# Kernel tuning notes

Measured on AMD Instinct MI355X. Metric: run time of the kernel, lower is better.

Reference implementation:

```python
import jax, jax.numpy as jnp
import numpy as np

N = 100000
E = 1600000
F_IN = 256
HID = 128
N_CLS = 2


def _glorot(k, shape):
    lim = float(np.sqrt(6.0 / (shape[0] + shape[1])))
    return jax.random.uniform(k, shape, jnp.float32, -lim, lim)


def setup_inputs() -> dict:
    key = jax.random.key(0)
    ks = jax.random.split(key, 10)
    x = jax.random.normal(ks[0], (N, F_IN), jnp.float32)
    edge_index = jax.random.randint(ks[1], (2, E), 0, N, dtype=jnp.int64)
    return {
        "x": x,
        "edge_index": edge_index,
        "W1": _glorot(ks[2], (F_IN, HID)), "b1": jnp.zeros((HID,), jnp.float32),
        "W2": _glorot(ks[3], (HID, HID)), "b2": jnp.zeros((HID,), jnp.float32),
        "W3": _glorot(ks[4], (HID, HID)), "b3": jnp.zeros((HID,), jnp.float32),
        "Wc": _glorot(ks[5], (HID, N_CLS)), "bc": jnp.zeros((N_CLS,), jnp.float32),
    }


def gcn_layer(x, W, b, src, dst, n):
    """PyG GCNConv: D^-1/2 (A+I) D^-1/2 X W + b with self-loops added."""
    xw = x @ W  # [N, H]
    # degree including the self-loop (all edge weights are 1)
    deg = jax.ops.segment_sum(jnp.ones((src.shape[0],), xw.dtype), dst,
                              num_segments=n) + 1.0
    dinv = jax.lax.rsqrt(deg)  # [N]
    norm = dinv[src] * dinv[dst]  # [E]
    msg = xw[src] * norm[:, None]  # [E, H] gathered+scaled messages
    out = jax.ops.segment_sum(msg, dst, num_segments=n)
    # self-loop contribution: norm = dinv[i]*dinv[i] = 1/deg[i]
    out = out + xw * (1.0 / deg)[:, None]
    return out + b


def reference(x, edge_index, W1, b1, W2, b2, W3, b3, Wc, bc):
    src, dst = edge_index[0], edge_index[1]
    h = jax.nn.relu(gcn_layer(x, W1, b1, src, dst, N))
    h = jax.nn.relu(gcn_layer(h, W2, b2, src, dst, N))  # dropout identity (eval)
    h = jax.nn.relu(gcn_layer(h, W3, b3, src, dst, N))
    logits = h @ Wc + bc  # [N, num_classes]
    return jax.nn.log_softmax(logits, axis=1)
```

## Files before the change

kernel.cpp:

```cpp
#include <hip/hip_runtime.h>
#include <hip/hip_bf16.h>
#include <cstdint>
#include <cstddef>

#define N_NODES 100000
#define N_EDGES 1600000
#define F_IN    256
#define HID     128
#define NB       ((N_NODES + 255) >> 8)
#define F3_CHUNK 7168
#define N_CHUNKS ((N_EDGES + F3_CHUNK - 1) / F3_CHUNK)

typedef __attribute__((ext_vector_type(8))) short  bf16x8;
typedef __attribute__((ext_vector_type(4))) float  f32x4;

static __device__ inline float bf2f(unsigned short u) {
    return __uint_as_float(((unsigned int)u) << 16);
}
static __device__ inline unsigned short f2bf(float f) {
    union { __hip_bfloat16 h; unsigned short u; } c;
    c.h = __float2bfloat16(f);
    return c.u;
}
static __device__ inline float lof(unsigned int w) { return __uint_as_float(w << 16); }
static __device__ inline float hif(unsigned int w) { return __uint_as_float(w & 0xffff0000u); }


__global__ __launch_bounds__(256) void zero_f_kernel(float* __restrict__ p, int n) {
    int i = blockIdx.x * 256 + threadIdx.x;
    if (i < n) p[i] = 0.f;
}


__global__ __launch_bounds__(256) void count_kernel(const int* __restrict__ dst,
                                                    int* __restrict__ ccnt, int nE) {
    __shared__ int c[NB];
    for (int i = threadIdx.x; i < NB; i += 256) c[i] = 0;
    __syncthreads();
    int base = blockIdx.x * F3_CHUNK;
    int m = min(F3_CHUNK, nE - base);
    for (int t = threadIdx.x; t < m; t += 256)
        atomicAdd(&c[dst[base + t] >> 8], 1);
    __syncthreads();
    for (int i = threadIdx.x; i < NB; i += 256)
        ccnt[i * N_CHUNKS + blockIdx.x] = c[i];
}


__global__ __launch_bounds__(256) void scanA_kernel(int* __restrict__ ccnt,
                                                    int* __restrict__ btot) {
    __shared__ int s[256];
    const int b = blockIdx.x;
    const int t = threadIdx.x;
    int v = (t < N_CHUNKS) ? ccnt[b * N_CHUNKS + t] : 0;
    s[t] = v;
    __syncthreads();
    for (int off = 1; off < 256; off <<= 1) {
        int add = (t >= off) ? s[t - off] : 0;
        __syncthreads();
        s[t] += add;
        __syncthreads();
    }
    if (t < N_CHUNKS) ccnt[b * N_CHUNKS + t] = s[t] - v;
    if (t == 255) btot[b] = s[255];
}


__global__ __launch_bounds__(512) void scanB_kernel(const int* __restrict__ btot,
                                                    int* __restrict__ bbase) {
    __shared__ int s[512];
    int t = threadIdx.x;
    int v = (t < NB) ? btot[t] : 0;
    s[t] = v;
    __syncthreads();
    for (int off = 1; off < 512; off <<= 1) {
        int add = (t >= off) ? s[t - off] : 0;
        __syncthreads();
        s[t] += add;
        __syncthreads();
    }
    if (t < NB) bbase[t] = s[t] - v;
    if (t == 0) bbase[NB] = N_EDGES;
}


__global__ __launch_bounds__(256) void stage_kernel(const int* __restrict__ src,
                                                    const int* __restrict__ dst,
                                                    const int* __restrict__ ccnt,
                                                    const int* __restrict__ bbase,
                                                    unsigned int* __restrict__ stg, int nE) {
    __shared__ int cnt[NB];
    __shared__ int bas[NB];
    const int chunk = blockIdx.x;
    for (int i = threadIdx.x; i < NB; i += 256) {
        cnt[i] = 0;
        bas[i] = bbase[i] + ccnt[i * N_CHUNKS + chunk];
    }
    __syncthreads();
    int base = chunk * F3_CHUNK;
    int m = min(F3_CHUNK, nE - base);
    for (int t = threadIdx.x; t < m; t += 256) {
        int d = dst[base + t];
        int s = src[base + t];
        int bkt = d >> 8;
        int k = atomicAdd(&cnt[bkt], 1);
        stg[bas[bkt] + k] = ((unsigned int)s << 8) | (unsigned int)(d & 255);
    }
}


__global__ __launch_bounds__(256) void bucket_finalize_kernel(
        const unsigned int* __restrict__ stg,
        const int* __restrict__ bbase,
        float* __restrict__ dinv,
        int* __restrict__ row_ptr,
        int* __restrict__ csr_src, int n) {
    __shared__ int c[256];
    __shared__ int s[256];
    __shared__ int lofs[256];
    const int b = blockIdx.x;
    const int t = threadIdx.x;
    const int beg = bbase[b], end = bbase[b + 1];

    c[t] = 0;
    __syncthreads();
    for (int i = beg + t; i < end; i += 256)
        atomicAdd(&c[stg[i] & 255u], 1);
    __syncthreads();

    const int node = b * 256 + t;
    const int myDeg = c[t];
    if (node < n) dinv[node] = rsqrtf((float)myDeg + 1.0f);

    s[t] = myDeg;
    __syncthreads();
    for (int off = 1; off < 256; off <<= 1) {
        int add = (t >= off) ? s[t - off] : 0;
        __syncthreads();
        s[t] += add;
        __syncthreads();
    }
    const int excl = s[t] - myDeg;
    lofs[t] = excl;
    if (node <= n) row_ptr[node] = beg + excl;

    __syncthreads();
    c[t] = 0;
    __syncthreads();
    for (int i = beg + t; i < end; i += 256) {
        unsigned int p = stg[i];
        int dl = (int)(p & 255u);
        int k = atomicAdd(&c[dl], 1);
        csr_src[beg + lofs[dl] + k] = (int)(p >> 8);
    }
}


static __device__ inline void blob_fill(const float* __restrict__ W,
                                        unsigned short* __restrict__ blob, int tid) {
    int lane = tid & 63;
    int c    = (tid >> 6) & 7;
    int s    = tid >> 9;
    int col  = c * 16 + (lane & 15);
    int kb   = s * 32 + (lane >> 4) * 8;
    bf16x8 o;
#pragma unroll
    for (int j = 0; j < 8; ++j)
        o[j] = (short)f2bf(W[(size_t)(kb + j) * HID + col]);
    *reinterpret_cast<bf16x8*>(blob + (size_t)tid * 8) = o;
}

__global__ __launch_bounds__(256) void prep_blob_all_kernel(const float* __restrict__ W1,
                                                            const float* __restrict__ W2,
                                                            const float* __restrict__ W3,
                                                            unsigned short* __restrict__ blob1,
                                                            unsigned short* __restrict__ blob2,
                                                            unsigned short* __restrict__ blob3) {
    int blk = blockIdx.x;
    if (blk < 16) {
        blob_fill(W1, blob1, blk * 256 + threadIdx.x);
    } else if (blk < 24) {
        blob_fill(W2, blob2, (blk - 16) * 256 + threadIdx.x);
    } else {
        blob_fill(W3, blob3, (blk - 24) * 256 + threadIdx.x);
    }
}


template <int K, bool IN_BF16>
__global__ __launch_bounds__(256) void mfma_gemm_kernel(const void* __restrict__ Xv,
                                                        const unsigned short* __restrict__ blob,
                                                        unsigned short* __restrict__ Y, int n) {
    constexpr int KSTEPS = K / 32;
    const int lane = threadIdx.x & 63;
    const int wave = threadIdx.x >> 6;
    const int rowbase = blockIdx.x * 128 + wave * 32;

    const int r0 = min(rowbase +      (lane & 15), n - 1);
    const int r1 = min(rowbase + 16 + (lane & 15), n - 1);
    const int koff = (lane >> 4) * 8;

    f32x4 acc0[8], acc1[8];
#pragma unroll
    for (int c = 0; c < 8; ++c) { acc0[c] = (f32x4)0.f; acc1[c] = (f32x4)0.f; }

#pragma unroll
    for (int s = 0; s < KSTEPS; ++s) {
        bf16x8 bfr[8];
#pragma unroll
        for (int c = 0; c < 8; ++c)
            bfr[c] = *reinterpret_cast<const bf16x8*>(blob + ((size_t)((s * 8 + c) * 64 + lane)) * 8);

        bf16x8 a0, a1;
        if (IN_BF16) {
            const unsigned short* Xb = (const unsigned short*)Xv;
            a0 = *reinterpret_cast<const bf16x8*>(Xb + (size_t)r0 * K + s * 32 + koff);
            a1 = *reinterpret_cast<const bf16x8*>(Xb + (size_t)r1 * K + s * 32 + koff);
        } else {
            const float* Xf = (const float*)Xv;
            const float4* p0 = reinterpret_cast<const float4*>(Xf + (size_t)r0 * K + s * 32 + koff);
            const float4* p1 = reinterpret_cast<const float4*>(Xf + (size_t)r1 * K + s * 32 + koff);
            float4 q0 = p0[0], q1 = p0[1], q2 = p1[0], q3 = p1[1];
            a0[0] = (short)f2bf(q0.x); a0[1] = (short)f2bf(q0.y);
            a0[2] = (short)f2bf(q0.z); a0[3] = (short)f2bf(q0.w);
            a0[4] = (short)f2bf(q1.x); a0[5] = (short)f2bf(q1.y);
            a0[6] = (short)f2bf(q1.z); a0[7] = (short)f2bf(q1.w);
            a1[0] = (short)f2bf(q2.x); a1[1] = (short)f2bf(q2.y);
            a1[2] = (short)f2bf(q2.z); a1[3] = (short)f2bf(q2.w);
            a1[4] = (short)f2bf(q3.x); a1[5] = (short)f2bf(q3.y);
            a1[6] = (short)f2bf(q3.z); a1[7] = (short)f2bf(q3.w);
        }

#pragma unroll
        for (int c = 0; c < 8; ++c) {
            acc0[c] = __builtin_amdgcn_mfma_f32_16x16x32_bf16(a0, bfr[c], acc0[c], 0, 0, 0);
            acc1[c] = __builtin_amdgcn_mfma_f32_16x16x32_bf16(a1, bfr[c], acc1[c], 0, 0, 0);
        }
    }

    const int col  = lane & 15;
    const int rsub = (lane >> 4) * 4;
#pragma unroll
    for (int c = 0; c < 8; ++c) {
#pragma unroll
        for (int r = 0; r < 4; ++r) {
            int row0 = rowbase + rsub + r;
            int row1 = rowbase + 16 + rsub + r;
            if (row0 < n) Y[(size_t)row0 * HID + c * 16 + col] = f2bf(acc0[c][r]);
            if (row1 < n) Y[(size_t)row1 * HID + c * 16 + col] = f2bf(acc1[c][r]);
        }
    }
}


template <bool CLS>
__global__ __launch_bounds__(256) void agg_gather_kernel(const unsigned short* __restrict__ xw,
                                                         const float* __restrict__ dinv,
                                                         const int* __restrict__ row_ptr,
                                                         const int* __restrict__ csr_src,
                                                         const float* __restrict__ b,
                                                         unsigned short* __restrict__ h,
                                                         const float* __restrict__ Wc,
                                                         const float* __restrict__ bc,
                                                         float* __restrict__ out, int n) {
    int v = (blockIdx.x * 256 + threadIdx.x) >> 6;
    if (v >= n) return;
    int lane = threadIdx.x & 63;

    int beg = __builtin_amdgcn_readfirstlane(row_ptr[v]);
    int end = __builtin_amdgcn_readfirstlane(row_ptr[v + 1]);

    const unsigned int* xw32 = (const unsigned int*)xw;
    float a0 = 0.f, a1 = 0.f;

    int j = beg;
    for (; j + 4 <= end; j += 4) {
        int s0 = __builtin_amdgcn_readfirstlane(csr_src[j + 0]);
        int s1 = __builtin_amdgcn_readfirstlane(csr_src[j + 1]);
        int s2 = __builtin_amdgcn_readfirstlane(csr_src[j + 2]);
        int s3 = __builtin_amdgcn_readfirstlane(csr_src[j + 3]);
        float d0 = dinv[s0], d1 = dinv[s1], d2 = dinv[s2], d3 = dinv[s3];
        unsigned int w0 = xw32[(size_t)s0 * 64 + lane];
        unsigned int w1 = xw32[(size_t)s1 * 64 + lane];
        unsigned int w2 = xw32[(size_t)s2 * 64 + lane];
        unsigned int w3 = xw32[(size_t)s3 * 64 + lane];
        a0 = fmaf(d0, lof(w0), a0); a1 = fmaf(d0, hif(w0), a1);
        a0 = fmaf(d1, lof(w1), a0); a1 = fmaf(d1, hif(w1), a1);
        a0 = fmaf(d2, lof(w2), a0); a1 = fmaf(d2, hif(w2), a1);
        a0 = fmaf(d3, lof(w3), a0); a1 = fmaf(d3, hif(w3), a1);
    }
    for (; j < end; ++j) {
        int s0 = __builtin_amdgcn_readfirstlane(csr_src[j]);
        float d0 = dinv[s0];
        unsigned int w0 = xw32[(size_t)s0 * 64 + lane];
        a0 = fmaf(d0, lof(w0), a0); a1 = fmaf(d0, hif(w0), a1);
    }

    float dv = dinv[v];
    unsigned int wv = xw32[(size_t)v * 64 + lane];
    float2 bb = *reinterpret_cast<const float2*>(b + 2 * lane);
    float s2v = dv * dv;
    float r0 = fmaxf(dv * a0 + s2v * lof(wv) + bb.x, 0.f);
    float r1 = fmaxf(dv * a1 + s2v * hif(wv) + bb.y, 0.f);

    if (!CLS) {
        unsigned int o = (unsigned int)f2bf(r0) | ((unsigned int)f2bf(r1) << 16);
        *reinterpret_cast<unsigned int*>(h + (size_t)v * HID + 2 * lane) = o;
    } else {
        float4 qw = *reinterpret_cast<const float4*>(Wc + 4 * lane);
        float p0 = r0 * qw.x + r1 * qw.z;
        float p1 = r0 * qw.y + r1 * qw.w;
#pragma unroll
        for (int off = 1; off < 64; off <<= 1) {
            p0 += __shfl_xor(p0, off);
            p1 += __shfl_xor(p1, off);
        }
        if (lane == 0) {
            float l0 = p0 + bc[0];
            float l1 = p1 + bc[1];
            float m = fmaxf(l0, l1);
            float lse = m + logf(expf(l0 - m) + expf(l1 - m));
            out[(size_t)v * 2 + 0] = l0 - lse;
            out[(size_t)v * 2 + 1] = l1 - lse;
        }
    }
}


static inline size_t align256(size_t x) { return (x + 255) & ~(size_t)255; }

extern "C" void kernel_launch(void* const* d_in, const int* in_sizes, int n_in,
                              void* d_out, int out_size, void* d_ws, size_t ws_size,
                              hipStream_t stream) {
    const float* x   = (const float*)d_in[0];
    const int*   ei  = (const int*)d_in[1];
    const float* W1  = (const float*)d_in[2];
    const float* b1  = (const float*)d_in[3];
    const float* W2  = (const float*)d_in[4];
    const float* b2  = (const float*)d_in[5];
    const float* W3  = (const float*)d_in[6];
    const float* b3  = (const float*)d_in[7];
    const float* Wc  = (const float*)d_in[8];
    const float* bc  = (const float*)d_in[9];
    float*       out = (float*)d_out;

    const int* src = ei;
    const int* dst = ei + N_EDGES;

    size_t off = 0;
    size_t o_dinv    = off; off = align256(off + (size_t)N_NODES * 4);
    size_t o_rowptr  = off; off = align256(off + (size_t)(N_NODES + 1) * 4);
    size_t o_ccnt    = off; off = align256(off + (size_t)NB * N_CHUNKS * 4);
    size_t o_btot    = off; off = align256(off + (size_t)NB * 4);
    size_t o_bbase   = off; off = align256(off + (size_t)(NB + 1) * 4);
    size_t o_csr     = off; off = align256(off + (size_t)N_EDGES * 4);
    size_t o_stg     = off; off = align256(off + (size_t)N_EDGES * 4);
    size_t o_blob1   = off; off = align256(off + (size_t)(F_IN / 32) * 8 * 64 * 8 * 2);
    size_t o_blob2   = off; off = align256(off + (size_t)(HID / 32) * 8 * 64 * 8 * 2);
    size_t o_blob3   = off; off = align256(off + (size_t)(HID / 32) * 8 * 64 * 8 * 2);
    size_t o_bufA    = off; off = align256(off + (size_t)N_NODES * HID * 2);
    size_t o_bufB    = off; off = align256(off + (size_t)N_NODES * HID * 2);
    size_t need = off;

    const int nThr = 256;
    const int gOut = (out_size + nThr - 1) / nThr;
    if (ws_size < need) {
        zero_f_kernel<<<gOut, nThr, 0, stream>>>(out, out_size);
        return;
    }

    char* ws = (char*)d_ws;
    float*          dinv    = (float*)(ws + o_dinv);
    int*            row_ptr = (int*)(ws + o_rowptr);
    int*            ccnt    = (int*)(ws + o_ccnt);
    int*            btot    = (int*)(ws + o_btot);
    int*            bbase   = (int*)(ws + o_bbase);
    int*            csr_src = (int*)(ws + o_csr);
    unsigned int*   stg     = (unsigned int*)(ws + o_stg);
    unsigned short* blob1   = (unsigned short*)(ws + o_blob1);
    unsigned short* blob2   = (unsigned short*)(ws + o_blob2);
    unsigned short* blob3   = (unsigned short*)(ws + o_blob3);
    unsigned short* bufA    = (unsigned short*)(ws + o_bufA);
    unsigned short* bufB    = (unsigned short*)(ws + o_bufB);

    const int gW = (N_NODES * 64 + nThr - 1) / nThr;
    const int gG = (N_NODES + 127) / 128;

    count_kernel<<<N_CHUNKS, nThr, 0, stream>>>(dst, ccnt, N_EDGES);
    scanA_kernel<<<NB, nThr, 0, stream>>>(ccnt, btot);
    scanB_kernel<<<1, 512, 0, stream>>>(btot, bbase);
    stage_kernel<<<N_CHUNKS, nThr, 0, stream>>>(src, dst, ccnt, bbase, stg, N_EDGES);
    bucket_finalize_kernel<<<NB, nThr, 0, stream>>>(stg, bbase, dinv, row_ptr, csr_src, N_NODES);

    prep_blob_all_kernel<<<32, nThr, 0, stream>>>(W1, W2, W3, blob1, blob2, blob3);

    mfma_gemm_kernel<F_IN, false><<<gG, nThr, 0, stream>>>(x, blob1, bufA, N_NODES);
    agg_gather_kernel<false><<<gW, nThr, 0, stream>>>(bufA, dinv, row_ptr, csr_src, b1,
                                                      bufB, nullptr, nullptr, nullptr, N_NODES);

    mfma_gemm_kernel<HID, true><<<gG, nThr, 0, stream>>>(bufB, blob2, bufA, N_NODES);
    agg_gather_kernel<false><<<gW, nThr, 0, stream>>>(bufA, dinv, row_ptr, csr_src, b2,
                                                      bufB, nullptr, nullptr, nullptr, N_NODES);

    mfma_gemm_kernel<HID, true><<<gG, nThr, 0, stream>>>(bufB, blob3, bufA, N_NODES);
    agg_gather_kernel<true><<<gW, nThr, 0, stream>>>(bufA, dinv, row_ptr, csr_src, b3,
                                                     nullptr, Wc, bc, out, N_NODES);
}
```

Before: 319.2 us.

## Slice features into XCD-affine column blocks with persistent work-queue gather

Stores hidden features in a sliced layout of eight 16-column slices, so each slice of the 100k-node matrix (about 3.2 MB) is meant to stay resident in one XCD's L2. The gather becomes a persistent kernel: each block reads its XCD id and pulls node groups from a per-slice atomic queue. Each block therefore aggregates only the slice local to its XCD, with 8 lanes per node. The classifier is split into its own kernel reading the sliced layout. The cost is eight times more row_ptr/csr_src/dinv traversal, more atomic queue contention, and an extra launch and HBM round trip for the final hidden state.

```diff
diff --git a/kernel.cpp b/kernel.cpp
--- a/kernel.cpp
+++ b/kernel.cpp
@@ -10,6 +10,9 @@
 #define NB       ((N_NODES + 255) >> 8)
 #define F3_CHUNK 7168
 #define N_CHUNKS ((N_EDGES + F3_CHUNK - 1) / F3_CHUNK)
+#define ITEMS_PER_SLICE (N_NODES / 32)
+#define QSTRIDE 16
+#define GATHER_BLOCKS 2048
 
 typedef __attribute__((ext_vector_type(8))) short  bf16x8;
 typedef __attribute__((ext_vector_type(4))) float  f32x4;
@@ -45,7 +48,6 @@
     for (int i = threadIdx.x; i < NB; i += 256)
         ccnt[i * N_CHUNKS + blockIdx.x] = c[i];
 }
-
 
 __global__ __launch_bounds__(256) void scanA_kernel(int* __restrict__ ccnt,
                                                     int* __restrict__ btot) {
@@ -67,9 +69,11 @@
 
 
 __global__ __launch_bounds__(512) void scanB_kernel(const int* __restrict__ btot,
-                                                    int* __restrict__ bbase) {
+                                                    int* __restrict__ bbase,
+                                                    int* __restrict__ qcAll) {
     __shared__ int s[512];
     int t = threadIdx.x;
+    if (t < 3 * 8 * QSTRIDE) qcAll[t] = 0;
     int v = (t < NB) ? btot[t] : 0;
     s[t] = v;
     __syncthreads();
@@ -82,7 +86,6 @@
     if (t < NB) bbase[t] = s[t] - v;
     if (t == 0) bbase[NB] = N_EDGES;
 }
-
 
 __global__ __launch_bounds__(256) void stage_kernel(const int* __restrict__ src,
                                                     const int* __restrict__ dst,
@@ -107,7 +110,6 @@
         stg[bas[bkt] + k] = ((unsigned int)s << 8) | (unsigned int)(d & 255);
     }
 }
-
 
 __global__ __launch_bounds__(256) void bucket_finalize_kernel(
         const unsigned int* __restrict__ stg,
@@ -214,8 +216,10 @@
         bf16x8 a0, a1;
         if (IN_BF16) {
             const unsigned short* Xb = (const unsigned short*)Xv;
-            a0 = *reinterpret_cast<const bf16x8*>(Xb + (size_t)r0 * K + s * 32 + koff);
-            a1 = *reinterpret_cast<const bf16x8*>(Xb + (size_t)r1 * K + s * 32 + koff);
+            const int c0 = s * 32 + koff;
+            const int sl = c0 >> 4, o16 = c0 & 15;
+            a0 = *reinterpret_cast<const bf16x8*>(Xb + ((size_t)(sl * N_NODES + r0)) * 16 + o16);
+            a1 = *reinterpret_cast<const bf16x8*>(Xb + ((size_t)(sl * N_NODES + r1)) * 16 + o16);
         } else {
             const float* Xf = (const float*)Xv;
             const float4* p0 = reinterpret_cast<const float4*>(Xf + (size_t)r0 * K + s * 32 + koff);
@@ -246,84 +250,106 @@
         for (int r = 0; r < 4; ++r) {
             int row0 = rowbase + rsub + r;
             int row1 = rowbase + 16 + rsub + r;
-            if (row0 < n) Y[(size_t)row0 * HID + c * 16 + col] = f2bf(acc0[c][r]);
-            if (row1 < n) Y[(size_t)row1 * HID + c * 16 + col] = f2bf(acc1[c][r]);
-        }
-    }
-}
-
-
-template <bool CLS>
-__global__ __launch_bounds__(256) void agg_gather_kernel(const unsigned short* __restrict__ xw,
-                                                         const float* __restrict__ dinv,
-                                                         const int* __restrict__ row_ptr,
-                                                         const int* __restrict__ csr_src,
-                                                         const float* __restrict__ b,
-                                                         unsigned short* __restrict__ h,
+            if (row0 < n) Y[((size_t)(c * N_NODES + row0)) * 16 + col] = f2bf(acc0[c][r]);
+            if (row1 < n) Y[((size_t)(c * N_NODES + row1)) * 16 + col] = f2bf(acc1[c][r]);
+        }
+    }
+}
+
+
+__global__ __launch_bounds__(256) void agg_gather_aff_kernel(
+        const unsigned short* __restrict__ xw,
+        const float* __restrict__ dinv,
+        const int* __restrict__ row_ptr,
+        const int* __restrict__ csr_src,
+        const float* __restrict__ b,
+        unsigned short* __restrict__ h,
+        int* __restrict__ qc, int n) {
+    __shared__ int s_item;
+    int xcd;
+    asm volatile("s_getreg_b32 %0, hwreg(20, 0, 32)" : "=s"(xcd));
+    xcd &= 7;
+    const int wave = threadIdx.x >> 6;
+    const int lane = threadIdx.x & 63;
+    const int grp  = lane >> 3;
+    const int l8   = lane & 7;
+
+    int attempt = 0;
+    while (attempt < 8) {
+        int q = (xcd + attempt) & 7;
+        if (threadIdx.x == 0) s_item = atomicAdd(&qc[q * QSTRIDE], 1);
+        __syncthreads();
+        int item = s_item;
+        __syncthreads();
+        if (item >= ITEMS_PER_SLICE) { ++attempt; continue; }
+
+        const unsigned int* xq = (const unsigned int*)xw + (size_t)q * n * 8;
+        const int v = item * 32 + wave * 8 + grp;
+        const int beg = row_ptr[v];
+        const int end = row_ptr[v + 1];
+
+        float a0 = 0.f, a1 = 0.f;
+        int j = beg;
+        for (; j + 2 <= end; j += 2) {
+            int s0 = csr_src[j];
+            int s1 = csr_src[j + 1];
+            float d0 = dinv[s0], d1 = dinv[s1];
+            unsigned int w0 = xq[(size_t)s0 * 8 + l8];
+            unsigned int w1 = xq[(size_t)s1 * 8 + l8];
+            a0 = fmaf(d0, lof(w0), a0); a1 = fmaf(d0, hif(w0), a1);
+            a0 = fmaf(d1, lof(w1), a0); a1 = fmaf(d1, hif(w1), a1);
+        }
+        if (j < end) {
+            int s0 = csr_src[j];
+            float d0 = dinv[s0];
+            unsigned int w0 = xq[(size_t)s0 * 8 + l8];
+            a0 = fmaf(d0, lof(w0), a0); a1 = fmaf(d0, hif(w0), a1);
+        }
+
+        float dv = dinv[v];
+        unsigned int wv = xq[(size_t)v * 8 + l8];
+        float2 bb = *reinterpret_cast<const float2*>(b + q * 16 + l8 * 2);
+        float s2v = dv * dv;
+        float r0 = fmaxf(dv * a0 + s2v * lof(wv) + bb.x, 0.f);
+        float r1 = fmaxf(dv * a1 + s2v * hif(wv) + bb.y, 0.f);
+        unsigned int* hq = (unsigned int*)h + (size_t)q * n * 8;
+        hq[(size_t)v * 8 + l8] = (unsigned int)f2bf(r0) | ((unsigned int)f2bf(r1) << 16);
+    }
+}
+
+
+__global__ __launch_bounds__(256) void classifier_kernel(const unsigned short* __restrict__ h,
                                                          const float* __restrict__ Wc,
                                                          const float* __restrict__ bc,
                                                          float* __restrict__ out, int n) {
-    int v = (blockIdx.x * 256 + threadIdx.x) >> 6;
-    if (v >= n) return;
-    int lane = threadIdx.x & 63;
-
-    int beg = __builtin_amdgcn_readfirstlane(row_ptr[v]);
-    int end = __builtin_amdgcn_readfirstlane(row_ptr[v + 1]);
-
-    const unsigned int* xw32 = (const unsigned int*)xw;
-    float a0 = 0.f, a1 = 0.f;
-
-    int j = beg;
-    for (; j + 4 <= end; j += 4) {
-        int s0 = __builtin_amdgcn_readfirstlane(csr_src[j + 0]);
-        int s1 = __builtin_amdgcn_readfirstlane(csr_src[j + 1]);
-        int s2 = __builtin_amdgcn_readfirstlane(csr_src[j + 2]);
-        int s3 = __builtin_amdgcn_readfirstlane(csr_src[j + 3]);
-        float d0 = dinv[s0], d1 = dinv[s1], d2 = dinv[s2], d3 = dinv[s3];
-        unsigned int w0 = xw32[(size_t)s0 * 64 + lane];
-        unsigned int w1 = xw32[(size_t)s1 * 64 + lane];
-        unsigned int w2 = xw32[(size_t)s2 * 64 + lane];
-        unsigned int w3 = xw32[(size_t)s3 * 64 + lane];
-        a0 = fmaf(d0, lof(w0), a0); a1 = fmaf(d0, hif(w0), a1);
-        a0 = fmaf(d1, lof(w1), a0); a1 = fmaf(d1, hif(w1), a1);
-        a0 = fmaf(d2, lof(w2), a0); a1 = fmaf(d2, hif(w2), a1);
-        a0 = fmaf(d3, lof(w3), a0); a1 = fmaf(d3, hif(w3), a1);
-    }
-    for (; j < end; ++j) {
-        int s0 = __builtin_amdgcn_readfirstlane(csr_src[j]);
-        float d0 = dinv[s0];
-        unsigned int w0 = xw32[(size_t)s0 * 64 + lane];
-        a0 = fmaf(d0, lof(w0), a0); a1 = fmaf(d0, hif(w0), a1);
-    }
-
-    float dv = dinv[v];
-    unsigned int wv = xw32[(size_t)v * 64 + lane];
-    float2 bb = *reinterpret_cast<const float2*>(b + 2 * lane);
-    float s2v = dv * dv;
-    float r0 = fmaxf(dv * a0 + s2v * lof(wv) + bb.x, 0.f);
-    float r1 = fmaxf(dv * a1 + s2v * hif(wv) + bb.y, 0.f);
-
-    if (!CLS) {
-        unsigned int o = (unsigned int)f2bf(r0) | ((unsigned int)f2bf(r1) << 16);
-        *reinterpret_cast<unsigned int*>(h + (size_t)v * HID + 2 * lane) = o;
-    } else {
-        float4 qw = *reinterpret_cast<const float4*>(Wc + 4 * lane);
-        float p0 = r0 * qw.x + r1 * qw.z;
-        float p1 = r0 * qw.y + r1 * qw.w;
-#pragma unroll
-        for (int off = 1; off < 64; off <<= 1) {
-            p0 += __shfl_xor(p0, off);
-            p1 += __shfl_xor(p1, off);
-        }
-        if (lane == 0) {
-            float l0 = p0 + bc[0];
-            float l1 = p1 + bc[1];
-            float m = fmaxf(l0, l1);
-            float lse = m + logf(expf(l0 - m) + expf(l1 - m));
-            out[(size_t)v * 2 + 0] = l0 - lse;
-            out[(size_t)v * 2 + 1] = l1 - lse;
-        }
-    }
+    __shared__ float wc0[HID], wc1[HID], bcs[2];
+    if (threadIdx.x < HID) {
+        wc0[threadIdx.x] = Wc[threadIdx.x * 2 + 0];
+        wc1[threadIdx.x] = Wc[threadIdx.x * 2 + 1];
+    }
+    if (threadIdx.x < 2) bcs[threadIdx.x] = bc[threadIdx.x];
+    __syncthreads();
+
+    int i = blockIdx.x * 256 + threadIdx.x;
+    if (i >= n) return;
+    float l0 = 0.f, l1 = 0.f;
+#pragma unroll
+    for (int sl = 0; sl < 8; ++sl) {
+        const bf16x8* p = reinterpret_cast<const bf16x8*>(h + ((size_t)(sl * n + i)) * 16);
+        bf16x8 qa = p[0], qb = p[1];
+#pragma unroll
+        for (int t = 0; t < 8; ++t) {
+            float va = bf2f((unsigned short)qa[t]);
+            float vb = bf2f((unsigned short)qb[t]);
+            l0 += va * wc0[sl * 16 + t] + vb * wc0[sl * 16 + 8 + t];
+            l1 += va * wc1[sl * 16 + t] + vb * wc1[sl * 16 + 8 + t];
+        }
+    }
+    l0 += bcs[0]; l1 += bcs[1];
+    float m = fmaxf(l0, l1);
+    float lse = m + logf(expf(l0 - m) + expf(l1 - m));
+    out[i * 2 + 0] = l0 - lse;
+    out[i * 2 + 1] = l1 - lse;
 }
 
 
@@ -353,6 +379,7 @@
     size_t o_ccnt    = off; off = align256(off + (size_t)NB * N_CHUNKS * 4);
     size_t o_btot    = off; off = align256(off + (size_t)NB * 4);
     size_t o_bbase   = off; off = align256(off + (size_t)(NB + 1) * 4);
+    size_t o_qc      = off; off = align256(off + (size_t)3 * 8 * QSTRIDE * 4);
     size_t o_csr     = off; off = align256(off + (size_t)N_EDGES * 4);
     size_t o_stg     = off; off = align256(off + (size_t)N_EDGES * 4);
     size_t o_blob1   = off; off = align256(off + (size_t)(F_IN / 32) * 8 * 64 * 8 * 2);
@@ -375,6 +402,7 @@
     int*            ccnt    = (int*)(ws + o_ccnt);
     int*            btot    = (int*)(ws + o_btot);
     int*            bbase   = (int*)(ws + o_bbase);
+    int*            qcAll   = (int*)(ws + o_qc);
     int*            csr_src = (int*)(ws + o_csr);
     unsigned int*   stg     = (unsigned int*)(ws + o_stg);
     unsigned short* blob1   = (unsigned short*)(ws + o_blob1);
@@ -383,26 +411,28 @@
     unsigned short* bufA    = (unsigned short*)(ws + o_bufA);
     unsigned short* bufB    = (unsigned short*)(ws + o_bufB);
 
-    const int gW = (N_NODES * 64 + nThr - 1) / nThr;
+    const int gN = (N_NODES + nThr - 1) / nThr;
     const int gG = (N_NODES + 127) / 128;
 
     count_kernel<<<N_CHUNKS, nThr, 0, stream>>>(dst, ccnt, N_EDGES);
     scanA_kernel<<<NB, nThr, 0, stream>>>(ccnt, btot);
-    scanB_kernel<<<1, 512, 0, stream>>>(btot, bbase);
+    scanB_kernel<<<1, 512, 0, stream>>>(btot, bbase, qcAll);
     stage_kernel<<<N_CHUNKS, nThr, 0, stream>>>(src, dst, ccnt, bbase, stg, N_EDGES);
     bucket_finalize_kernel<<<NB, nThr, 0, stream>>>(stg, bbase, dinv, row_ptr, csr_src, N_NODES);
 
     prep_blob_all_kernel<<<32, nThr, 0, stream>>>(W1, W2, W3, blob1, blob2, blob3);
 
     mfma_gemm_kernel<F_IN, false><<<gG, nThr, 0, stream>>>(x, blob1, bufA, N_NODES);
-    agg_gather_kernel<false><<<gW, nThr, 0, stream>>>(bufA, dinv, row_ptr, csr_src, b1,
-                                                      bufB, nullptr, nullptr, nullptr, N_NODES);
+    agg_gather_aff_kernel<<<GATHER_BLOCKS, nThr, 0, stream>>>(bufA, dinv, row_ptr, csr_src,
+                                                              b1, bufB, qcAll, N_NODES);
 
     mfma_gemm_kernel<HID, true><<<gG, nThr, 0, stream>>>(bufB, blob2, bufA, N_NODES);
-    agg_gather_kernel<false><<<gW, nThr, 0, stream>>>(bufA, dinv, row_ptr, csr_src, b2,
-                                                      bufB, nullptr, nullptr, nullptr, N_NODES);
+    agg_gather_aff_kernel<<<GATHER_BLOCKS, nThr, 0, stream>>>(bufA, dinv, row_ptr, csr_src,
+                                                              b2, bufB, qcAll + 8 * QSTRIDE, N_NODES);
 
     mfma_gemm_kernel<HID, true><<<gG, nThr, 0, stream>>>(bufB, blob3, bufA, N_NODES);
-    agg_gather_kernel<true><<<gW, nThr, 0, stream>>>(bufA, dinv, row_ptr, csr_src, b3,
-                                                     nullptr, Wc, bc, out, N_NODES);
-}
+    agg_gather_aff_kernel<<<GATHER_BLOCKS, nThr, 0, stream>>>(bufA, dinv, row_ptr, csr_src,
+                                                              b3, bufB, qcAll + 16 * QSTRIDE, N_NODES);
+
+    classifier_kernel<<<gN, nThr, 0, stream>>>(bufB, Wc, bc, out, N_NODES);
+}
```

Result: slower. 674.1 us (+111.2%).
